# Performance work log

Measured on AMD Instinct MI355X. Metric: run time of the kernel, lower is better.

## Reference

```python
import jax, jax.numpy as jnp
import numpy as np

B, T, S, C, E, H = 4, 2048, 2048, 256, 512, 8
D = E // H
SCALE = E ** (-0.5)


def setup_inputs() -> dict:
    key = jax.random.key(0)
    ks = jax.random.split(key, 12)
    x = jax.random.normal(ks[0], (B, T, C), dtype=jnp.float32)
    context = jax.random.normal(ks[1], (B, S, E), dtype=jnp.float32)
    pad_mask = jax.random.randint(ks[2], (B, T, S), 0, 2) == 1
    p = 0.02
    # Conv1d kernel_size=1 weights stored squeezed: [out_ch, in_ch]
    w_in = jax.random.normal(ks[3], (E, C), dtype=jnp.float32) * p
    b_in = jnp.zeros((E,), dtype=jnp.float32)
    wq = jax.random.normal(ks[4], (E, E), dtype=jnp.float32) * p
    bq = jnp.zeros((E,), dtype=jnp.float32)
    wk = jax.random.normal(ks[5], (E, E), dtype=jnp.float32) * p
    bk = jnp.zeros((E,), dtype=jnp.float32)
    wv = jax.random.normal(ks[6], (E, E), dtype=jnp.float32) * p
    bv = jnp.zeros((E,), dtype=jnp.float32)
    w_out = jax.random.normal(ks[7], (C, E), dtype=jnp.float32) * p
    b_out = jnp.zeros((C,), dtype=jnp.float32)
    return {"x": x, "context": context, "pad_mask": pad_mask,
            "w_in": w_in, "b_in": b_in, "wq": wq, "bq": bq,
            "wk": wk, "bk": bk, "wv": wv, "bv": bv,
            "w_out": w_out, "b_out": b_out}


def reference(x, context, pad_mask, w_in, b_in, wq, bq, wk, bk, wv, bv, w_out, b_out):
    # proj_in: Conv1d k=1 == per-token linear on channel dim. [B,T,C] -> [B,T,E]
    xe = jnp.einsum('btc,ec->bte', x, w_in) + b_in
    Q = (xe @ wq.T + bq).reshape(B, T, H, D)       # query tokens
    K = (context @ wk.T + bk).reshape(B, S, H, D)  # key tokens
    V = (context @ wv.T + bv).reshape(B, S, H, D)
    att = jnp.einsum('bihd,bjhd->bhij', Q, K) * SCALE  # [B,H,T,S]
    att = jnp.where(pad_mask[:, None, :, :], jnp.float32(-1e9), att)
    att = jax.nn.softmax(att, axis=-1)
    out = jnp.einsum('bhij,bjhd->bihd', att, V).reshape(B, T, E)
    # proj_out: Conv1d k=1, [B,T,E] -> [B,T,C]
    out = jnp.einsum('bte,ce->btc', out, w_out) + b_out
    return out
```

## Files before the change

kernel.cpp:

```cpp
#include <hip/hip_runtime.h>
#include <cstdint>
#include <cstddef>

#define Bb 4
#define Tt 2048
#define Ssz 2048
#define Cc 256
#define Ee 512
#define Hh 8

typedef short bf8 __attribute__((ext_vector_type(8)));
typedef float f4 __attribute__((ext_vector_type(4)));

__device__ __forceinline__ unsigned short f2bf(float x) {
  unsigned int u = __float_as_uint(x);
  u += 0x7fffu + ((u >> 16) & 1u);
  return (unsigned short)(u >> 16);
}

__device__ __forceinline__ bf8 cvt8(float4 a, float4 b) {
  bf8 r;
  r[0] = (short)f2bf(a.x); r[1] = (short)f2bf(a.y);
  r[2] = (short)f2bf(a.z); r[3] = (short)f2bf(a.w);
  r[4] = (short)f2bf(b.x); r[5] = (short)f2bf(b.y);
  r[6] = (short)f2bf(b.z); r[7] = (short)f2bf(b.w);
  return r;
}

__global__ __launch_bounds__(256) void prep(const int* __restrict__ mask,
                                            const float* __restrict__ w_in,
                                            const float* __restrict__ b_in,
                                            const float* __restrict__ wq,
                                            const float* __restrict__ bq,
                                            const float* __restrict__ wk,
                                            const float* __restrict__ wv,
                                            const float* __restrict__ wo,
                                            unsigned int* __restrict__ mp,
                                            unsigned short* __restrict__ wkvb,
                                            unsigned short* __restrict__ wob,
                                            unsigned short* __restrict__ wqin,
                                            float* __restrict__ bqinb, float qsc) {
  __shared__ unsigned short sh[128][72];
  const int bid = blockIdx.x, tid = threadIdx.x;
  if (bid < 2048) {
    int i = bid * 256 + tid;
    const int4* src = (const int4*)mask + (size_t)i * 8;
    unsigned int w = 0;
#pragma unroll
    for (int k = 0; k < 8; k++) {
      int4 v = src[k];
      w |= (unsigned int)(v.x != 0) << (k * 4);
      w |= (unsigned int)(v.y != 0) << (k * 4 + 1);
      w |= (unsigned int)(v.z != 0) << (k * 4 + 2);
      w |= (unsigned int)(v.w != 0) << (k * 4 + 3);
    }
    mp[i] = w;
  } else if (bid < 2560) {
    int i = (bid - 2048) * 256 + tid;
    const float* s = (i < 65536) ? wk : wv;
    int off = (i < 65536) ? i : i - 65536;
    float4 v = ((const float4*)s)[off];
    ushort4 o;
    o.x = f2bf(v.x); o.y = f2bf(v.y); o.z = f2bf(v.z); o.w = f2bf(v.w);
    ((ushort4*)wkvb)[i] = o;
  } else if (bid < 2688) {
    int i = (bid - 2560) * 256 + tid;
    float4 v = ((const float4*)wo)[i];
    ushort4 o;
    o.x = f2bf(v.x); o.y = f2bf(v.y); o.z = f2bf(v.z); o.w = f2bf(v.w);
    ((ushort4*)wob)[i] = o;
  } else if (bid < 2720) {
    const int idx = bid - 2688;
    const int m0 = (idx & 7) * 64, n0 = (idx >> 3) * 64;
    unsigned short (*As)[72] = (unsigned short (*)[72]) & sh[0][0];
    unsigned short (*Bs)[72] = (unsigned short (*)[72]) & sh[64][0];
    const int wave = tid >> 6, lane = tid & 63;
    const int lrow = lane & 15, quad = lane >> 4;
    const int wm = (wave >> 1) * 32, wn = (wave & 1) * 32;
    const int arow = tid >> 3, ac = tid & 7;
    f4 acc[2][2];
#pragma unroll
    for (int i = 0; i < 2; i++)
#pragma unroll
      for (int j = 0; j < 2; j++) {
        f4 z = {0.f, 0.f, 0.f, 0.f};
        acc[i][j] = z;
      }
    for (int kt = 0; kt < 8; kt++) {
#pragma unroll
      for (int i = 0; i < 2; i++) {
        int row = arow + i * 32;
        const float* src = wq + (size_t)(m0 + row) * Ee + kt * 64 + ac * 8;
        float4 v0 = *(const float4*)src, v1 = *(const float4*)(src + 4);
        bf8 av;
        av[0] = (short)f2bf(v0.x * qsc); av[1] = (short)f2bf(v0.y * qsc);
        av[2] = (short)f2bf(v0.z * qsc); av[3] = (short)f2bf(v0.w * qsc);
        av[4] = (short)f2bf(v1.x * qsc); av[5] = (short)f2bf(v1.y * qsc);
        av[6] = (short)f2bf(v1.z * qsc); av[7] = (short)f2bf(v1.w * qsc);
        *(bf8*)&As[row][ac * 8] = av;
        int c = n0 + row;
        bf8 bv;
#pragma unroll
        for (int k = 0; k < 8; k++)
          bv[k] = (short)f2bf(w_in[(size_t)(kt * 64 + ac * 8 + k) * Cc + c]);
        *(bf8*)&Bs[row][ac * 8] = bv;
      }
      __syncthreads();
#pragma unroll
      for (int kk = 0; kk < 2; kk++) {
        bf8 af[2], bff[2];
#pragma unroll
        for (int i = 0; i < 2; i++) af[i] = *(const bf8*)&As[wm + i * 16 + lrow][kk * 32 + quad * 8];
#pragma unroll
        for (int j = 0; j < 2; j++) bff[j] = *(const bf8*)&Bs[wn + j * 16 + lrow][kk * 32 + quad * 8];
#pragma unroll
        for (int i = 0; i < 2; i++)
#pragma unroll
          for (int j = 0; j < 2; j++)
            acc[i][j] = __builtin_amdgcn_mfma_f32_16x16x32_bf16(af[i], bff[j], acc[i][j], 0, 0, 0);
      }
      __syncthreads();
    }
#pragma unroll
    for (int j = 0; j < 2; j++)
#pragma unroll
      for (int i = 0; i < 2; i++)
#pragma unroll
        for (int r = 0; r < 4; r++)
          wqin[(size_t)(m0 + wm + i * 16 + quad * 4 + r) * Cc + n0 + wn + j * 16 + lrow] =
              f2bf(acc[i][j][r]);
  } else {
    const int o = (bid - 2720) * 32 + (tid >> 3);
    const int k0 = (tid & 7) * 64;
    float s = 0.f;
#pragma unroll
    for (int i = 0; i < 16; i++) {
      float4 w = *(const float4*)(wq + (size_t)o * Ee + k0 + i * 4);
      float4 bb = *(const float4*)(b_in + k0 + i * 4);
      s += w.x * bb.x + w.y * bb.y + w.z * bb.z + w.w * bb.w;
    }
    s += __shfl_xor(s, 1);
    s += __shfl_xor(s, 2);
    s += __shfl_xor(s, 4);
    if ((tid & 7) == 0) bqinb[o] = (s + bq[o]) * qsc;
  }
}

__global__ __launch_bounds__(256) void qkv(const float* __restrict__ x,
                                           const float* __restrict__ ctx,
                                           const unsigned short* __restrict__ wqin,
                                           const float* __restrict__ bqinb,
                                           const unsigned short* __restrict__ wkv,
                                           const float* __restrict__ bk,
                                           const float* __restrict__ bv,
                                           unsigned short* __restrict__ Qb,
                                           unsigned short* __restrict__ Kb,
                                           unsigned short* __restrict__ Vt) {
  __shared__ unsigned short As[128][72];
  __shared__ unsigned short Bs[128][72];
  const int bid = blockIdx.x, tid = threadIdx.x;
  const bool isQ = bid < 256;
  const int idx = isQ ? bid : bid - 256;
  const int m0 = (idx & 63) * 128;
  const int n0 = (idx >> 6) * 128;
  const int K = isQ ? 256 : 512;
  const float* A = isQ ? x : ctx;
  const unsigned short* Bt = isQ ? wqin : wkv;

  const int wave = tid >> 6, lane = tid & 63;
  const int lrow = lane & 15, quad = lane >> 4;
  const int wm = (wave >> 1) * 64, wn = (wave & 1) * 64;
  const int arow = tid >> 3, ac = tid & 7;

  f4 acc[4][4];
#pragma unroll
  for (int i = 0; i < 4; i++)
#pragma unroll
    for (int j = 0; j < 4; j++) {
      f4 z = {0.f, 0.f, 0.f, 0.f};
      acc[i][j] = z;
    }

  float4 ap0[4], ap1[4];
  bf8 bpre[4];
#pragma unroll
  for (int i = 0; i < 4; i++) {
    const float* src = A + (size_t)(m0 + arow + i * 32) * K + ac * 8;
    ap0[i] = *(const float4*)src;
    ap1[i] = *(const float4*)(src + 4);
    bpre[i] = *(const bf8*)(Bt + (size_t)(n0 + arow + i * 32) * K + ac * 8);
  }

  const int nkt = K >> 6;
  for (int kt = 0; kt < nkt; ++kt) {
#pragma unroll
    for (int i = 0; i < 4; i++) {
      *(bf8*)&As[arow + i * 32][ac * 8] = cvt8(ap0[i], ap1[i]);
      *(bf8*)&Bs[arow + i * 32][ac * 8] = bpre[i];
    }
    __syncthreads();
    if (kt + 1 < nkt) {
      int k0 = (kt + 1) << 6;
#pragma unroll
      for (int i = 0; i < 4; i++) {
        const float* src = A + (size_t)(m0 + arow + i * 32) * K + k0 + ac * 8;
        ap0[i] = *(const float4*)src;
        ap1[i] = *(const float4*)(src + 4);
        bpre[i] = *(const bf8*)(Bt + (size_t)(n0 + arow + i * 32) * K + k0 + ac * 8);
      }
    }
#pragma unroll
    for (int kk = 0; kk < 2; kk++) {
      bf8 af[4], bff[4];
#pragma unroll
      for (int i = 0; i < 4; i++)
        af[i] = *(const bf8*)&As[wm + i * 16 + lrow][kk * 32 + quad * 8];
#pragma unroll
      for (int j = 0; j < 4; j++)
        bff[j] = *(const bf8*)&Bs[wn + j * 16 + lrow][kk * 32 + quad * 8];
#pragma unroll
      for (int i = 0; i < 4; i++)
#pragma unroll
        for (int j = 0; j < 4; j++)
          acc[i][j] = __builtin_amdgcn_mfma_f32_16x16x32_bf16(af[i], bff[j],
                                                              acc[i][j], 0, 0, 0);
    }
    __syncthreads();
  }

  if (isQ) {
#pragma unroll
    for (int j = 0; j < 4; j++) {
      int col = n0 + wn + j * 16 + lrow;
      float bvv = bqinb[col];
#pragma unroll
      for (int i = 0; i < 4; i++)
#pragma unroll
        for (int r = 0; r < 4; r++)
          Qb[(size_t)(m0 + wm + i * 16 + quad * 4 + r) * Ee + col] =
              f2bf(acc[i][j][r] + bvv);
    }
  } else if (n0 < 512) {
#pragma unroll
    for (int j = 0; j < 4; j++) {
      int col = n0 + wn + j * 16 + lrow;
      float bvv = bk[col];
#pragma unroll
      for (int i = 0; i < 4; i++)
#pragma unroll
        for (int r = 0; r < 4; r++)
          Kb[(size_t)(m0 + wm + i * 16 + quad * 4 + r) * Ee + col] =
              f2bf(acc[i][j][r] + bvv);
    }
  } else {
#pragma unroll
    for (int j = 0; j < 4; j++) {
      int d = n0 - 512 + wn + j * 16 + lrow;
      int h = d >> 6, dd = d & 63;
      float bvv = bv[d];
#pragma unroll
      for (int i = 0; i < 4; i++) {
        int tok = m0 + wm + i * 16 + quad * 4;
        int b = tok >> 11, sl = tok & 2047;
        ushort4 pk;
        pk.x = f2bf(acc[i][j][0] + bvv);
        pk.y = f2bf(acc[i][j][1] + bvv);
        pk.z = f2bf(acc[i][j][2] + bvv);
        pk.w = f2bf(acc[i][j][3] + bvv);
        *(ushort4*)(Vt + (size_t)((b * Hh + h) * 64 + dd) * Ssz + sl) = pk;
      }
    }
  }
}

template <bool OUT_BF16, int BM, int BN, int WGM>
__global__ __launch_bounds__(256) void gemm_bt(const unsigned short* __restrict__ A,
                                               const unsigned short* __restrict__ Bt,
                                               const float* __restrict__ bias0,
                                               void* __restrict__ Cout,
                                               int M, int N, int K) {
  constexpr int WGN = 4 / WGM;
  constexpr int MI = BM / (WGM * 16);
  constexpr int NJ = BN / (WGN * 16);
  constexpr int NA = BM / 32;
  constexpr int NB = BN / 32;
  __shared__ unsigned short As[BM][72];
  __shared__ unsigned short Bs[BN][72];
  const int tid = threadIdx.x;
  const int wave = tid >> 6, lane = tid & 63;
  const int lrow = lane & 15, quad = lane >> 4;
  const int wm = (wave / WGN) * (BM / WGM);
  const int wn = (wave % WGN) * (BN / WGN);
  const int m0 = blockIdx.x * BM, n0 = blockIdx.y * BN;
  const int arow = tid >> 3, ac = tid & 7;

  f4 acc[MI][NJ];
#pragma unroll
  for (int i = 0; i < MI; i++)
#pragma unroll
    for (int j = 0; j < NJ; j++) {
      f4 z = {0.f, 0.f, 0.f, 0.f};
      acc[i][j] = z;
    }

  bf8 apre[NA], bpre[NB];
#pragma unroll
  for (int i = 0; i < NA; i++)
    apre[i] = *(const bf8*)(A + (size_t)(m0 + arow + i * 32) * K + ac * 8);
#pragma unroll
  for (int i = 0; i < NB; i++)
    bpre[i] = *(const bf8*)(Bt + (size_t)(n0 + arow + i * 32) * K + ac * 8);

  const int nkt = K >> 6;
  for (int kt = 0; kt < nkt; ++kt) {
#pragma unroll
    for (int i = 0; i < NA; i++) *(bf8*)&As[arow + i * 32][ac * 8] = apre[i];
#pragma unroll
    for (int i = 0; i < NB; i++) *(bf8*)&Bs[arow + i * 32][ac * 8] = bpre[i];
    __syncthreads();
    if (kt + 1 < nkt) {
      int k0 = (kt + 1) << 6;
#pragma unroll
      for (int i = 0; i < NA; i++)
        apre[i] = *(const bf8*)(A + (size_t)(m0 + arow + i * 32) * K + k0 + ac * 8);
#pragma unroll
      for (int i = 0; i < NB; i++)
        bpre[i] = *(const bf8*)(Bt + (size_t)(n0 + arow + i * 32) * K + k0 + ac * 8);
    }
#pragma unroll
    for (int kk = 0; kk < 2; kk++) {
      bf8 af[MI], bff[NJ];
#pragma unroll
      for (int i = 0; i < MI; i++)
        af[i] = *(const bf8*)&As[wm + i * 16 + lrow][kk * 32 + quad * 8];
#pragma unroll
      for (int j = 0; j < NJ; j++)
        bff[j] = *(const bf8*)&Bs[wn + j * 16 + lrow][kk * 32 + quad * 8];
#pragma unroll
      for (int i = 0; i < MI; i++)
#pragma unroll
        for (int j = 0; j < NJ; j++)
          acc[i][j] = __builtin_amdgcn_mfma_f32_16x16x32_bf16(af[i], bff[j],
                                                              acc[i][j], 0, 0, 0);
    }
    __syncthreads();
  }

#pragma unroll
  for (int j = 0; j < NJ; j++) {
    int col = n0 + wn + j * 16 + lrow;
    float bvv = bias0 ? bias0[col] : 0.f;
#pragma unroll
    for (int i = 0; i < MI; i++) {
#pragma unroll
      for (int r = 0; r < 4; r++) {
        int row = m0 + wm + i * 16 + quad * 4 + r;
        float v = acc[i][j][r] + bvv;
        if (OUT_BF16)
          ((unsigned short*)Cout)[(size_t)row * N + col] = f2bf(v);
        else
          ((float*)Cout)[(size_t)row * N + col] = v;
      }
    }
  }
}

__global__ __launch_bounds__(256) void attn(const unsigned short* __restrict__ Q,
                                            const unsigned short* __restrict__ K,
                                            const unsigned short* __restrict__ Vt,
                                            const unsigned int* __restrict__ mp,
                                            unsigned short* __restrict__ O) {
  __shared__ unsigned short Ks[2][64][72];
  __shared__ unsigned short Vts[2][64][72];
  __shared__ unsigned short Ps[256][72];
  const int tid = threadIdx.x;
  const int wave = tid >> 6, lane = tid & 63;
  const int lrow = lane & 15, quad = lane >> 4;
  const int b = blockIdx.z, h = blockIdx.y, t0 = blockIdx.x * 256;
  const int arow = tid >> 3, ac = tid & 7;
  const int wm = wave * 64;

#pragma unroll
  for (int i = 0; i < 8; i++) {
    int row = arow + i * 32;
    *(bf8*)&Ps[row][ac * 8] =
        *(const bf8*)(Q + (size_t)(b * Tt + t0 + row) * Ee + h * 64 + ac * 8);
  }
  __syncthreads();
  bf8 qf[4][2];
#pragma unroll
  for (int mi = 0; mi < 4; mi++) {
    qf[mi][0] = *(const bf8*)&Ps[wm + mi * 16 + lrow][quad * 8];
    qf[mi][1] = *(const bf8*)&Ps[wm + mi * 16 + lrow][32 + quad * 8];
  }

  f4 oacc[4][4];
  f4 dacc[4];
#pragma unroll
  for (int mi = 0; mi < 4; mi++) {
    f4 z = {0.f, 0.f, 0.f, 0.f};
    dacc[mi] = z;
#pragma unroll
    for (int j = 0; j < 4; j++) oacc[mi][j] = z;
  }
  bf8 ones;
#pragma unroll
  for (int k = 0; k < 8; k++) ones[k] = (short)0x3F80;

  const unsigned short* Kbase = K + (size_t)b * Ssz * Ee + h * 64;
  const unsigned short* Vbase = Vt + (size_t)((b * Hh + h) * 64) * Ssz;
  const unsigned int* mrow[4];
#pragma unroll
  for (int mi = 0; mi < 4; mi++)
    mrow[mi] = mp + (size_t)(b * Tt + t0 + wm + mi * 16 + lrow) * 64;

  bf8 kreg[2], vreg[2];
#pragma unroll
  for (int i = 0; i < 2; i++) {
    int row = arow + i * 32;
    kreg[i] = *(const bf8*)(Kbase + (size_t)row * Ee + ac * 8);
    vreg[i] = *(const bf8*)(Vbase + (size_t)row * Ssz + ac * 8);
  }

  int buf = 0;
  for (int s0 = 0; s0 < Ssz; s0 += 64) {
#pragma unroll
    for (int i = 0; i < 2; i++) {
      int row = arow + i * 32;
      *(bf8*)&Ks[buf][row][ac * 8] = kreg[i];
      *(bf8*)&Vts[buf][row][ac * 8] = vreg[i];
    }
    __syncthreads();
    if (s0 + 64 < Ssz) {
#pragma unroll
      for (int i = 0; i < 2; i++) {
        int row = arow + i * 32;
        kreg[i] = *(const bf8*)(Kbase + (size_t)(s0 + 64 + row) * Ee + ac * 8);
        vreg[i] = *(const bf8*)(Vbase + (size_t)row * Ssz + s0 + 64 + ac * 8);
      }
    }
    uint2 mw[4];
#pragma unroll
    for (int mi = 0; mi < 4; mi++) mw[mi] = *(const uint2*)(mrow[mi] + (s0 >> 5));

#pragma unroll
    for (int sf = 0; sf < 4; sf++) {
      bf8 kf0 = *(const bf8*)&Ks[buf][sf * 16 + lrow][quad * 8];
      bf8 kf1 = *(const bf8*)&Ks[buf][sf * 16 + lrow][32 + quad * 8];
      f4 sa[4];
#pragma unroll
      for (int mi = 0; mi < 4; mi++) {
        f4 z = {0.f, 0.f, 0.f, 0.f};
        sa[mi] = z;
        sa[mi] = __builtin_amdgcn_mfma_f32_16x16x32_bf16(kf0, qf[mi][0], sa[mi], 0, 0, 0);
        sa[mi] = __builtin_amdgcn_mfma_f32_16x16x32_bf16(kf1, qf[mi][1], sa[mi], 0, 0, 0);
      }
#pragma unroll
      for (int mi = 0; mi < 4; mi++) {
        const unsigned int w = (sf >= 2) ? mw[mi].y : mw[mi].x;
        ushort4 pk;
#pragma unroll
        for (int r = 0; r < 4; r++) {
          const unsigned int bit = (sf & 1) * 16 + quad * 4 + r;
          float e = __builtin_amdgcn_exp2f(sa[mi][r]);
          float p = ((w >> bit) & 1u) ? 0.f : e;
          unsigned short pb = (unsigned short)(__float_as_uint(p) >> 16);
          if (r == 0) pk.x = pb;
          else if (r == 1) pk.y = pb;
          else if (r == 2) pk.z = pb;
          else pk.w = pb;
        }
        *(ushort4*)&Ps[wm + mi * 16 + lrow][sf * 16 + quad * 4] = pk;
      }
    }
#pragma unroll
    for (int kk = 0; kk < 2; kk++) {
      bf8 pf[4];
#pragma unroll
      for (int mi = 0; mi < 4; mi++) {
        pf[mi] = *(const bf8*)&Ps[wm + mi * 16 + lrow][kk * 32 + quad * 8];
        dacc[mi] = __builtin_amdgcn_mfma_f32_16x16x32_bf16(pf[mi], ones, dacc[mi], 0, 0, 0);
      }
#pragma unroll
      for (int j = 0; j < 4; j++) {
        bf8 vf = *(const bf8*)&Vts[buf][j * 16 + lrow][kk * 32 + quad * 8];
#pragma unroll
        for (int mi = 0; mi < 4; mi++)
          oacc[mi][j] = __builtin_amdgcn_mfma_f32_16x16x32_bf16(pf[mi], vf, oacc[mi][j], 0, 0, 0);
      }
    }
    buf ^= 1;
  }

#pragma unroll
  for (int mi = 0; mi < 4; mi++) {
#pragma unroll
    for (int r = 0; r < 4; r++) {
      float inv = 1.0f / dacc[mi][r];
      int row = b * Tt + t0 + wm + mi * 16 + quad * 4 + r;
#pragma unroll
      for (int j = 0; j < 4; j++)
        O[(size_t)row * Ee + h * 64 + j * 16 + lrow] = f2bf(oacc[mi][j][r] * inv);
    }
  }
}

extern "C" void kernel_launch(void* const* d_in, const int* in_sizes, int n_in,
                              void* d_out, int out_size, void* d_ws, size_t ws_size,
                              hipStream_t stream) {
  const float* x    = (const float*)d_in[0];
  const float* ctx  = (const float*)d_in[1];
  const int*   mask = (const int*)d_in[2];
  const float* w_in = (const float*)d_in[3];
  const float* b_in = (const float*)d_in[4];
  const float* wq   = (const float*)d_in[5];
  const float* bq   = (const float*)d_in[6];
  const float* wk   = (const float*)d_in[7];
  const float* bk   = (const float*)d_in[8];
  const float* wv   = (const float*)d_in[9];
  const float* bv   = (const float*)d_in[10];
  const float* wo   = (const float*)d_in[11];
  const float* bo   = (const float*)d_in[12];

  const float qsc = 0.04419417382415922f * 1.4426950408889634f;

  unsigned short* ws = (unsigned short*)d_ws;
  unsigned int*   maskp = (unsigned int*)ws;
  unsigned short* wkvb  = ws + 1048576;
  unsigned short* wob   = ws + 1572864;
  unsigned short* wqin  = ws + 1703936;
  float*          bqinb = (float*)(ws + 1835008);
  unsigned short* Qb    = ws + 1836032;
  unsigned short* Kb    = ws + 6030336;
  unsigned short* Vtb   = ws + 10224640;
  unsigned short* Ob    = ws + 14418944;

  prep<<<2736, 256, 0, stream>>>(mask, w_in, b_in, wq, bq, wk, wv, wo,
                                 maskp, wkvb, wob, wqin, bqinb, qsc);
  qkv<<<768, 256, 0, stream>>>(x, ctx, wqin, bqinb, wkvb, bk, bv, Qb, Kb, Vtb);
  attn<<<dim3(8, 8, 4), 256, 0, stream>>>(Qb, Kb, Vtb, maskp, Ob);
  gemm_bt<false, 64, 64, 2><<<dim3(128, 4), 256, 0, stream>>>(
      Ob, wob, bo, d_out, 8192, 256, 512);
}
```

Before: 264.0 us.

## Halve attention tile to 128 rows, drop LDS double buffer, move mask packing into qkv

```diff
diff --git a/kernel.cpp b/kernel.cpp
--- a/kernel.cpp
+++ b/kernel.cpp
@@ -27,50 +27,35 @@
   return r;
 }
 
-__global__ __launch_bounds__(256) void prep(const int* __restrict__ mask,
-                                            const float* __restrict__ w_in,
+__global__ __launch_bounds__(256) void prep(const float* __restrict__ w_in,
                                             const float* __restrict__ b_in,
                                             const float* __restrict__ wq,
                                             const float* __restrict__ bq,
                                             const float* __restrict__ wk,
                                             const float* __restrict__ wv,
                                             const float* __restrict__ wo,
-                                            unsigned int* __restrict__ mp,
                                             unsigned short* __restrict__ wkvb,
                                             unsigned short* __restrict__ wob,
                                             unsigned short* __restrict__ wqin,
                                             float* __restrict__ bqinb, float qsc) {
   __shared__ unsigned short sh[128][72];
   const int bid = blockIdx.x, tid = threadIdx.x;
-  if (bid < 2048) {
+  if (bid < 512) {
     int i = bid * 256 + tid;
-    const int4* src = (const int4*)mask + (size_t)i * 8;
-    unsigned int w = 0;
-#pragma unroll
-    for (int k = 0; k < 8; k++) {
-      int4 v = src[k];
-      w |= (unsigned int)(v.x != 0) << (k * 4);
-      w |= (unsigned int)(v.y != 0) << (k * 4 + 1);
-      w |= (unsigned int)(v.z != 0) << (k * 4 + 2);
-      w |= (unsigned int)(v.w != 0) << (k * 4 + 3);
-    }
-    mp[i] = w;
-  } else if (bid < 2560) {
-    int i = (bid - 2048) * 256 + tid;
     const float* s = (i < 65536) ? wk : wv;
     int off = (i < 65536) ? i : i - 65536;
     float4 v = ((const float4*)s)[off];
     ushort4 o;
     o.x = f2bf(v.x); o.y = f2bf(v.y); o.z = f2bf(v.z); o.w = f2bf(v.w);
     ((ushort4*)wkvb)[i] = o;
-  } else if (bid < 2688) {
-    int i = (bid - 2560) * 256 + tid;
+  } else if (bid < 640) {
+    int i = (bid - 512) * 256 + tid;
     float4 v = ((const float4*)wo)[i];
     ushort4 o;
     o.x = f2bf(v.x); o.y = f2bf(v.y); o.z = f2bf(v.z); o.w = f2bf(v.w);
     ((ushort4*)wob)[i] = o;
-  } else if (bid < 2720) {
-    const int idx = bid - 2688;
+  } else if (bid < 672) {
+    const int idx = bid - 640;
     const int m0 = (idx & 7) * 64, n0 = (idx >> 3) * 64;
     unsigned short (*As)[72] = (unsigned short (*)[72]) & sh[0][0];
     unsigned short (*Bs)[72] = (unsigned short (*)[72]) & sh[64][0];
@@ -130,7 +115,7 @@
           wqin[(size_t)(m0 + wm + i * 16 + quad * 4 + r) * Cc + n0 + wn + j * 16 + lrow] =
               f2bf(acc[i][j][r]);
   } else {
-    const int o = (bid - 2720) * 32 + (tid >> 3);
+    const int o = (bid - 672) * 32 + (tid >> 3);
     const int k0 = (tid & 7) * 64;
     float s = 0.f;
 #pragma unroll
@@ -155,10 +140,27 @@
                                            const float* __restrict__ bv,
                                            unsigned short* __restrict__ Qb,
                                            unsigned short* __restrict__ Kb,
-                                           unsigned short* __restrict__ Vt) {
+                                           unsigned short* __restrict__ Vt,
+                                           const int* __restrict__ mask,
+                                           unsigned int* __restrict__ mp) {
   __shared__ unsigned short As[128][72];
   __shared__ unsigned short Bs[128][72];
   const int bid = blockIdx.x, tid = threadIdx.x;
+  if (bid >= 768) {
+    int i = (bid - 768) * 256 + tid;
+    const int4* src = (const int4*)mask + (size_t)i * 8;
+    unsigned int w = 0;
+#pragma unroll
+    for (int k = 0; k < 8; k++) {
+      int4 v = src[k];
+      w |= (unsigned int)(v.x != 0) << (k * 4);
+      w |= (unsigned int)(v.y != 0) << (k * 4 + 1);
+      w |= (unsigned int)(v.z != 0) << (k * 4 + 2);
+      w |= (unsigned int)(v.w != 0) << (k * 4 + 3);
+    }
+    mp[i] = w;
+    return;
+  }
   const bool isQ = bid < 256;
   const int idx = isQ ? bid : bid - 256;
   const int m0 = (idx & 63) * 128;
@@ -370,34 +372,36 @@
                                             const unsigned short* __restrict__ Vt,
                                             const unsigned int* __restrict__ mp,
                                             unsigned short* __restrict__ O) {
-  __shared__ unsigned short Ks[2][64][72];
-  __shared__ unsigned short Vts[2][64][72];
-  __shared__ unsigned short Ps[256][72];
+  __shared__ unsigned short Ks[64][72];
+  __shared__ unsigned short Vts[64][72];
+  __shared__ unsigned short Ps[128][72];
   const int tid = threadIdx.x;
   const int wave = tid >> 6, lane = tid & 63;
   const int lrow = lane & 15, quad = lane >> 4;
-  const int b = blockIdx.z, h = blockIdx.y, t0 = blockIdx.x * 256;
+  const int bid = blockIdx.x;
+  const int bh = bid & 31, b = bh >> 3, h = bh & 7;
+  const int t0 = (bid >> 5) * 128;
   const int arow = tid >> 3, ac = tid & 7;
-  const int wm = wave * 64;
-
-#pragma unroll
-  for (int i = 0; i < 8; i++) {
+  const int wm = wave * 32;
+
+#pragma unroll
+  for (int i = 0; i < 4; i++) {
     int row = arow + i * 32;
     *(bf8*)&Ps[row][ac * 8] =
         *(const bf8*)(Q + (size_t)(b * Tt + t0 + row) * Ee + h * 64 + ac * 8);
   }
   __syncthreads();
-  bf8 qf[4][2];
-#pragma unroll
-  for (int mi = 0; mi < 4; mi++) {
+  bf8 qf[2][2];
+#pragma unroll
+  for (int mi = 0; mi < 2; mi++) {
     qf[mi][0] = *(const bf8*)&Ps[wm + mi * 16 + lrow][quad * 8];
     qf[mi][1] = *(const bf8*)&Ps[wm + mi * 16 + lrow][32 + quad * 8];
   }
 
-  f4 oacc[4][4];
-  f4 dacc[4];
-#pragma unroll
-  for (int mi = 0; mi < 4; mi++) {
+  f4 oacc[2][4];
+  f4 dacc[2];
+#pragma unroll
+  for (int mi = 0; mi < 2; mi++) {
     f4 z = {0.f, 0.f, 0.f, 0.f};
     dacc[mi] = z;
 #pragma unroll
@@ -409,10 +413,8 @@
 
   const unsigned short* Kbase = K + (size_t)b * Ssz * Ee + h * 64;
   const unsigned short* Vbase = Vt + (size_t)((b * Hh + h) * 64) * Ssz;
-  const unsigned int* mrow[4];
-#pragma unroll
-  for (int mi = 0; mi < 4; mi++)
-    mrow[mi] = mp + (size_t)(b * Tt + t0 + wm + mi * 16 + lrow) * 64;
+  const unsigned int* mrow0 = mp + (size_t)(b * Tt + t0 + wm + lrow) * 64;
+  const unsigned int* mrow1 = mp + (size_t)(b * Tt + t0 + wm + 16 + lrow) * 64;
 
   bf8 kreg[2], vreg[2];
 #pragma unroll
@@ -422,13 +424,13 @@
     vreg[i] = *(const bf8*)(Vbase + (size_t)row * Ssz + ac * 8);
   }
 
-  int buf = 0;
   for (int s0 = 0; s0 < Ssz; s0 += 64) {
+    __syncthreads();
 #pragma unroll
     for (int i = 0; i < 2; i++) {
       int row = arow + i * 32;
-      *(bf8*)&Ks[buf][row][ac * 8] = kreg[i];
-      *(bf8*)&Vts[buf][row][ac * 8] = vreg[i];
+      *(bf8*)&Ks[row][ac * 8] = kreg[i];
+      *(bf8*)&Vts[row][ac * 8] = vreg[i];
     }
     __syncthreads();
     if (s0 + 64 < Ssz) {
@@ -439,25 +441,24 @@
         vreg[i] = *(const bf8*)(Vbase + (size_t)row * Ssz + s0 + 64 + ac * 8);
       }
     }
-    uint2 mw[4];
-#pragma unroll
-    for (int mi = 0; mi < 4; mi++) mw[mi] = *(const uint2*)(mrow[mi] + (s0 >> 5));
+    const uint2 mw0 = *(const uint2*)(mrow0 + (s0 >> 5));
+    const uint2 mw1 = *(const uint2*)(mrow1 + (s0 >> 5));
 
 #pragma unroll
     for (int sf = 0; sf < 4; sf++) {
-      bf8 kf0 = *(const bf8*)&Ks[buf][sf * 16 + lrow][quad * 8];
-      bf8 kf1 = *(const bf8*)&Ks[buf][sf * 16 + lrow][32 + quad * 8];
-      f4 sa[4];
-#pragma unroll
-      for (int mi = 0; mi < 4; mi++) {
-        f4 z = {0.f, 0.f, 0.f, 0.f};
-        sa[mi] = z;
-        sa[mi] = __builtin_amdgcn_mfma_f32_16x16x32_bf16(kf0, qf[mi][0], sa[mi], 0, 0, 0);
-        sa[mi] = __builtin_amdgcn_mfma_f32_16x16x32_bf16(kf1, qf[mi][1], sa[mi], 0, 0, 0);
-      }
-#pragma unroll
-      for (int mi = 0; mi < 4; mi++) {
-        const unsigned int w = (sf >= 2) ? mw[mi].y : mw[mi].x;
+      bf8 kf0 = *(const bf8*)&Ks[sf * 16 + lrow][quad * 8];
+      bf8 kf1 = *(const bf8*)&Ks[sf * 16 + lrow][32 + quad * 8];
+      f4 sa[2];
+      f4 z = {0.f, 0.f, 0.f, 0.f};
+      sa[0] = z; sa[1] = z;
+      sa[0] = __builtin_amdgcn_mfma_f32_16x16x32_bf16(kf0, qf[0][0], sa[0], 0, 0, 0);
+      sa[0] = __builtin_amdgcn_mfma_f32_16x16x32_bf16(kf1, qf[0][1], sa[0], 0, 0, 0);
+      sa[1] = __builtin_amdgcn_mfma_f32_16x16x32_bf16(kf0, qf[1][0], sa[1], 0, 0, 0);
+      sa[1] = __builtin_amdgcn_mfma_f32_16x16x32_bf16(kf1, qf[1][1], sa[1], 0, 0, 0);
+#pragma unroll
+      for (int mi = 0; mi < 2; mi++) {
+        const uint2 mw = mi ? mw1 : mw0;
+        const unsigned int w = (sf >= 2) ? mw.y : mw.x;
         ushort4 pk;
 #pragma unroll
         for (int r = 0; r < 4; r++) {
@@ -475,25 +476,24 @@
     }
 #pragma unroll
     for (int kk = 0; kk < 2; kk++) {
-      bf8 pf[4];
-#pragma unroll
-      for (int mi = 0; mi < 4; mi++) {
+      bf8 pf[2];
+#pragma unroll
+      for (int mi = 0; mi < 2; mi++) {
         pf[mi] = *(const bf8*)&Ps[wm + mi * 16 + lrow][kk * 32 + quad * 8];
         dacc[mi] = __builtin_amdgcn_mfma_f32_16x16x32_bf16(pf[mi], ones, dacc[mi], 0, 0, 0);
       }
 #pragma unroll
       for (int j = 0; j < 4; j++) {
-        bf8 vf = *(const bf8*)&Vts[buf][j * 16 + lrow][kk * 32 + quad * 8];
-#pragma unroll
-        for (int mi = 0; mi < 4; mi++)
+        bf8 vf = *(const bf8*)&Vts[j * 16 + lrow][kk * 32 + quad * 8];
+#pragma unroll
+        for (int mi = 0; mi < 2; mi++)
           oacc[mi][j] = __builtin_amdgcn_mfma_f32_16x16x32_bf16(pf[mi], vf, oacc[mi][j], 0, 0, 0);
       }
     }
-    buf ^= 1;
-  }
-
-#pragma unroll
-  for (int mi = 0; mi < 4; mi++) {
+  }
+
+#pragma unroll
+  for (int mi = 0; mi < 2; mi++) {
 #pragma unroll
     for (int r = 0; r < 4; r++) {
       float inv = 1.0f / dacc[mi][r];
@@ -535,10 +535,11 @@
   unsigned short* Vtb   = ws + 10224640;
   unsigned short* Ob    = ws + 14418944;
 
-  prep<<<2736, 256, 0, stream>>>(mask, w_in, b_in, wq, bq, wk, wv, wo,
-                                 maskp, wkvb, wob, wqin, bqinb, qsc);
-  qkv<<<768, 256, 0, stream>>>(x, ctx, wqin, bqinb, wkvb, bk, bv, Qb, Kb, Vtb);
-  attn<<<dim3(8, 8, 4), 256, 0, stream>>>(Qb, Kb, Vtb, maskp, Ob);
+  prep<<<688, 256, 0, stream>>>(w_in, b_in, wq, bq, wk, wv, wo,
+                                wkvb, wob, wqin, bqinb, qsc);
+  qkv<<<2816, 256, 0, stream>>>(x, ctx, wqin, bqinb, wkvb, bk, bv, Qb, Kb, Vtb,
+                                mask, maskp);
+  attn<<<512, 256, 0, stream>>>(Qb, Kb, Vtb, maskp, Ob);
   gemm_bt<false, 64, 64, 2><<<dim3(128, 4), 256, 0, stream>>>(
       Ob, wob, bo, d_out, 8192, 256, 512);
 }
```

Result: faster. 237.5 us (-10.0%).
